# Optimization experiments

Measured on AMD Instinct MI355X. Metric: run time of the kernel, lower is better.

The kernel has to match this reference:

```python
import jax, jax.numpy as jnp
import numpy as np

HEADS = 8

def group_conv1x1(x, w, heads):
    # x: (B, Cin, H, W); w: (Cout, Cin//heads, 1, 1) grouped 1x1 conv, no bias
    B, Cin, H, W = x.shape
    Cout = w.shape[0]
    xg = x.reshape(B, heads, Cin // heads, H * W)
    wg = w[:, :, 0, 0].reshape(heads, Cout // heads, Cin // heads)
    out = jnp.einsum('hoc,bhcl->bhol', wg, xg)
    return out.reshape(B, Cout, H, W)

def sine_pe(d_model, length):
    # standard transformer sin/cos encoding, laid out as (d_model, length)
    pos = jnp.arange(length, dtype=jnp.float32)
    i = jnp.arange(0, d_model, 2, dtype=jnp.float32)
    div = jnp.exp(-(jnp.log(10000.0)) * i / d_model)
    ang = div[:, None] * pos[None, :]            # (d/2, L)
    pe = jnp.zeros((d_model, length), dtype=jnp.float32)
    pe = pe.at[0::2].set(jnp.sin(ang)).at[1::2].set(jnp.cos(ang))
    return pe

def setup_inputs() -> dict:
    key = jax.random.key(0)
    k0, k1, k2, k3 = jax.random.split(key, 4)
    B, Cin, H, W = 16, 256, 32, 32
    Cout, heads = 256, HEADS
    fan_out = Cout  # kaiming_normal fan_out for 1x1 conv = Cout*1*1
    std = np.sqrt(2.0 / fan_out)
    x = jax.random.normal(k0, (B, Cin, H, W), dtype=jnp.float32)
    wq = jax.random.normal(k1, (Cout, Cin // heads, 1, 1), dtype=jnp.float32) * std
    wk = jax.random.normal(k2, (Cout, Cin // heads, 1, 1), dtype=jnp.float32) * std
    wv = jax.random.normal(k3, (Cout, Cin // heads, 1, 1), dtype=jnp.float32) * std
    return {"x": x, "wq": wq, "wk": wk, "wv": wv}

def reference(x, wq, wk, wv):
    B, Cin, H, W = x.shape
    Cout = wq.shape[0]
    heads = HEADS
    dh = Cout // heads
    L = H * W

    q = group_conv1x1(x, wq, heads)              # (B, Cout, H, W)
    k = group_conv1x1(x, wk, heads)
    v = group_conv1x1(x, wv, heads)

    # sine positional encoding added to keys over flattened spatial positions
    k = k.reshape(B, Cout, L) + sine_pe(Cout, L)[None]

    q = q.reshape(B, heads, dh, L)               # (B, h, dh, L)
    k = k.reshape(B, heads, dh, L)
    v = v.reshape(B, heads, dh, L)

    scores = jnp.einsum('bhdq,bhdk->bhqk', q, k)  # (B, h, L, L) -- no sqrt(d) scaling, as in source
    attn = jax.nn.softmax(scores, axis=-1)
    out = jnp.einsum('bhqk,bhdk->bhdq', attn, v)  # (B, h, dh, L)
    return out.reshape(B, Cout, H, W)
```

## Files before the change

### kernel.cpp

```cpp
#include <hip/hip_runtime.h>

#define LL   1024
#define BHD  128
#define LOG2E 1.44269504088896340736f

typedef unsigned int       uint;
typedef unsigned short     ushort;
typedef unsigned long long ull;

typedef __attribute__((ext_vector_type(8)))  __bf16          bf16x8;
typedef __attribute__((ext_vector_type(8)))  unsigned short  u16x8;
typedef __attribute__((ext_vector_type(4)))  unsigned short  u16x4;
typedef __attribute__((ext_vector_type(4)))  uint            ui32x4;
typedef __attribute__((ext_vector_type(4)))  float           f32x4;
typedef __attribute__((ext_vector_type(16))) float           f32x16;

static __device__ __forceinline__ ushort f2bf(float f){
  union {float f; uint u;} v; v.f = f;
  uint u = v.u + 0x7fffu + ((v.u >> 16) & 1u);
  return (ushort)(u >> 16);
}
static __device__ __forceinline__ uint pack2(float a, float b){
  return (uint)f2bf(a) | ((uint)f2bf(b) << 16);
}
static __device__ __forceinline__ uint packtrunc(float a, float b){
  union {float f; uint u;} x, y; x.f = a; y.f = b;
  return __builtin_amdgcn_perm(y.u, x.u, 0x07060302u);
}
static __device__ __forceinline__ bf16x8 ld_frag(const ushort* p){
  u16x8 t = *(const u16x8*)p;
  return __builtin_bit_cast(bf16x8, t);
}
static __device__ __forceinline__ bf16x8 ld_frag64(const ushort* p){
  u16x4 a = *(const u16x4*)p;
  u16x4 b = *(const u16x4*)(p + 4);
  u16x8 t;
  t[0]=a[0]; t[1]=a[1]; t[2]=a[2]; t[3]=a[3];
  t[4]=b[0]; t[5]=b[1]; t[6]=b[2]; t[7]=b[3];
  return __builtin_bit_cast(bf16x8, t);
}

static __device__ __forceinline__ bool sniff_is_bf16(const uint* xw, int tid, int* cnt){
  uint w = xw[tid & 255];
  uint e = (w >> 7) & 0xFFu;
  bool hit = (e >= 118u) && (e <= 132u);
  ull b = __ballot(hit);
  if ((tid & 63) == 0) cnt[tid >> 6] = __popcll(b);
  __syncthreads();
  bool r = (cnt[0] + cnt[1] + cnt[2] + cnt[3]) > 128;
  __syncthreads();
  return r;
}

__global__ __launch_bounds__(256) void qkv_kernel(
    const void* __restrict__ xr,
    const void* __restrict__ wqr,
    const void* __restrict__ wkr,
    const void* __restrict__ wvr,
    ushort* __restrict__ Qt, ushort* __restrict__ Kt, ushort* __restrict__ Vt)
{
  const int bh   = blockIdx.x;
  const int lt   = blockIdx.y;
  const int tid  = threadIdx.x;
  const int wave = tid >> 6;
  const int lane = tid & 63;
  const int l16  = lane & 15;
  const int quad = lane >> 4;
  const int lbase = lt * 128;

  __shared__ int cnt[4];
  __shared__ __align__(16) uint xsd[128][20];

  const bool is_bf = sniff_is_bf16((const uint*)xr, tid, cnt);

  {
    const int cp = tid & 15, lg = tid >> 4;
    const size_t rb = (size_t)(bh*32 + 2*cp)*LL + lbase + lg*8;
    uint dw[8];
    if (is_bf){
      u16x8 e = *(const u16x8*)((const ushort*)xr + rb);
      u16x8 o = *(const u16x8*)((const ushort*)xr + rb + LL);
      #pragma unroll
      for (int j = 0; j < 8; ++j) dw[j] = (uint)e[j] | ((uint)o[j] << 16);
    } else {
      const float* xf = (const float*)xr;
      float4 e0 = *(const float4*)(xf + rb);
      float4 e1 = *(const float4*)(xf + rb + 4);
      float4 o0 = *(const float4*)(xf + rb + LL);
      float4 o1 = *(const float4*)(xf + rb + LL + 4);
      dw[0]=pack2(e0.x,o0.x); dw[1]=pack2(e0.y,o0.y);
      dw[2]=pack2(e0.z,o0.z); dw[3]=pack2(e0.w,o0.w);
      dw[4]=pack2(e1.x,o1.x); dw[5]=pack2(e1.y,o1.y);
      dw[6]=pack2(e1.z,o1.z); dw[7]=pack2(e1.w,o1.w);
    }
    #pragma unroll
    for (int j = 0; j < 8; ++j) xsd[lg*8 + j][cp] = dw[j];
  }
  __syncthreads();

  const void* wsrc[3] = {wqr, wkr, wvr};
  bf16x8 bw[3][2];
  #pragma unroll
  for (int p = 0; p < 3; ++p)
    #pragma unroll
    for (int nh = 0; nh < 2; ++nh){
      const int row = (bh & 7)*32 + nh*16 + l16;
      if (is_bf){
        bw[p][nh] = ld_frag((const ushort*)wsrc[p] + (size_t)row*32 + quad*8);
      } else {
        const float* wf = (const float*)wsrc[p] + (size_t)row*32 + quad*8;
        float4 f0 = *(const float4*)wf, f1 = *(const float4*)(wf + 4);
        u16x8 t;
        t[0]=f2bf(f0.x); t[1]=f2bf(f0.y); t[2]=f2bf(f0.z); t[3]=f2bf(f0.w);
        t[4]=f2bf(f1.x); t[5]=f2bf(f1.y); t[6]=f2bf(f1.z); t[7]=f2bf(f1.w);
        bw[p][nh] = __builtin_bit_cast(bf16x8, t);
      }
    }

  bf16x8 ax[2];
  #pragma unroll
  for (int mt = 0; mt < 2; ++mt)
    ax[mt] = __builtin_bit_cast(bf16x8,
               *(const ui32x4*)&xsd[wave*32 + mt*16 + l16][quad*4]);

  const f32x4 z = {0.f,0.f,0.f,0.f};
  f32x4 dq[2][2], dk[2][2], dv[2][2];
  #pragma unroll
  for (int mt = 0; mt < 2; ++mt)
    #pragma unroll
    for (int nh = 0; nh < 2; ++nh){
      dq[mt][nh] = __builtin_amdgcn_mfma_f32_16x16x32_bf16(ax[mt], bw[0][nh], z, 0,0,0);
      dk[mt][nh] = __builtin_amdgcn_mfma_f32_16x16x32_bf16(ax[mt], bw[1][nh], z, 0,0,0);
      dv[nh][mt] = __builtin_amdgcn_mfma_f32_16x16x32_bf16(bw[2][nh], ax[mt], z, 0,0,0);
    }

  #pragma unroll
  for (int mt = 0; mt < 2; ++mt)
    #pragma unroll
    for (int nh = 0; nh < 2; ++nh)
      #pragma unroll
      for (int r = 0; r < 4; ++r){
        const int l = lbase + wave*32 + mt*16 + quad*4 + r;
        const int d = nh*16 + l16;
        Qt[((size_t)bh*LL + l)*32 + d] = f2bf(dq[mt][nh][r]);
      }
  #pragma unroll
  for (int mt = 0; mt < 2; ++mt)
    #pragma unroll
    for (int nh = 0; nh < 2; ++nh){
      const int d = nh*16 + l16;
      const int c = (bh & 7)*32 + d;
      const float freq = __expf(-0.03597789207f * (float)(c & ~1));
      #pragma unroll
      for (int r = 0; r < 4; ++r){
        const int l = lbase + wave*32 + mt*16 + quad*4 + r;
        const float ang = freq * (float)l;
        const float pe  = (c & 1) ? __cosf(ang) : __sinf(ang);
        Kt[((size_t)bh*LL + l)*32 + d] = f2bf((dk[mt][nh][r] + pe) * LOG2E);
      }
    }
  #pragma unroll
  for (int dh = 0; dh < 2; ++dh)
    #pragma unroll
    for (int mt = 0; mt < 2; ++mt)
      #pragma unroll
      for (int r = 0; r < 4; ++r){
        const int d = dh*16 + quad*4 + r;
        const int l = lbase + wave*32 + mt*16 + l16;
        Vt[((size_t)(bh*32 + d))*LL + l] = f2bf(dv[dh][mt][r]);
      }
}

__global__ __launch_bounds__(256, 4) void attn_kernel(
    const void*   __restrict__ xr,
    const ushort* __restrict__ Qt,
    const ushort* __restrict__ Kt,
    const ushort* __restrict__ Vt,
    void* __restrict__ out)
{
  const int bh  = blockIdx.x;
  const int qt  = blockIdx.y;
  const int tid = threadIdx.x;
  const int wave = tid >> 6;
  const int lane = tid & 63;
  const int q32  = lane & 31;
  const int h    = lane >> 5;

  __shared__ int cnt[4];
  __shared__ __align__(16) ushort Ks[64][40];
  __shared__ __align__(16) ushort Vs[32][68];

  const bool is_bf = sniff_is_bf16((const uint*)xr, tid, cnt);

  const int qg = qt*128 + wave*32 + q32;
  const ushort* qrow = Qt + ((size_t)bh*LL + qg)*32;
  bf16x8 bq0 = ld_frag(qrow + h*8);
  bf16x8 bq1 = ld_frag(qrow + 16 + h*8);

  const int skey = tid >> 2, sseg = tid & 3;
  const int sp = (sseg + (skey >> 2)) & 3;
  const ushort* kg = Kt + ((size_t)(bh*LL + skey))*32 + sseg*8;
  ushort* kw = &Ks[skey][sp*8];
  const int sd = tid >> 3, sg = tid & 7;
  const ushort* vg = Vt + ((size_t)(bh*32 + sd))*LL + sg*8;
  ushort* vw = &Vs[sd][sg*8];

  const int rot = (q32 >> 2) & 3;
  const ushort* ka0 = &Ks[q32][((h + rot) & 3)*8];
  const ushort* ka1 = &Ks[q32][((2 + h + rot) & 3)*8];
  const ushort* vr  = &Vs[q32][h*8];

  f32x16 O = {};
  float rsum = 0.f;

  u16x8 kreg = *(const u16x8*)kg;
  u16x8 vreg = *(const u16x8*)vg;

  for (int kt = 0; kt < 16; ++kt){
    __syncthreads();
    *(u16x8*)kw = kreg;
    { u16x4 lo, hi;
      lo[0]=vreg[0]; lo[1]=vreg[1]; lo[2]=vreg[2]; lo[3]=vreg[3];
      hi[0]=vreg[4]; hi[1]=vreg[5]; hi[2]=vreg[6]; hi[3]=vreg[7];
      *(u16x4*)vw = lo; *(u16x4*)(vw + 4) = hi; }
    __syncthreads();
    if (kt < 15){
      kreg = *(const u16x8*)(kg + (size_t)(kt+1)*64*32);
      vreg = *(const u16x8*)(vg + (kt+1)*64);
    }

    f32x16 st[2];
    #pragma unroll
    for (int t = 0; t < 2; ++t){
      bf16x8 a0 = ld_frag(ka0 + t*32*40);
      bf16x8 a1 = ld_frag(ka1 + t*32*40);
      f32x16 zz = {};
      f32x16 s  = __builtin_amdgcn_mfma_f32_32x32x16_bf16(a0, bq0, zz, 0,0,0);
      st[t]     = __builtin_amdgcn_mfma_f32_32x32x16_bf16(a1, bq1, s,  0,0,0);
    }

    uint pr[2][8];
    #pragma unroll
    for (int t = 0; t < 2; ++t)
      #pragma unroll
      for (int zi = 0; zi < 8; ++zi){
        float p0 = __builtin_amdgcn_exp2f(st[t][2*zi]);
        float p1 = __builtin_amdgcn_exp2f(st[t][2*zi+1]);
        rsum += p0 + p1;
        pr[t][zi] = packtrunc(p0, p1);
      }

    #pragma unroll
    for (int c = 0; c < 4; ++c){
      const int t = c >> 1, g0 = 4*(c & 1);
      uint s0 = h ? pr[t][g0+0] : pr[t][g0+2];
      uint s1 = h ? pr[t][g0+1] : pr[t][g0+3];
      uint r0 = (uint)__shfl_xor((int)s0, 32);
      uint r1 = (uint)__shfl_xor((int)s1, 32);
      ui32x4 pb;
      pb[0] = h ? r0 : pr[t][g0+0];
      pb[1] = h ? r1 : pr[t][g0+1];
      pb[2] = h ? pr[t][g0+2] : r0;
      pb[3] = h ? pr[t][g0+3] : r1;
      bf16x8 va = ld_frag64(vr + c*16);
      O = __builtin_amdgcn_mfma_f32_32x32x16_bf16(
            va, __builtin_bit_cast(bf16x8, pb), O, 0,0,0);
    }
  }

  rsum += __shfl_xor(rsum, 32);
  const float inv = 1.f / rsum;

  #pragma unroll
  for (int reg = 0; reg < 16; ++reg){
    const int d = (reg & 3) + 8*(reg >> 2) + 4*h;
    const float v = O[reg] * inv;
    const size_t off = ((size_t)(bh*32 + d))*LL + qg;
    if (is_bf) ((ushort*)out)[off] = f2bf(v);
    else       ((float*)out)[off]  = v;
  }
}

extern "C" void kernel_launch(void* const* d_in, const int* in_sizes, int n_in,
                              void* d_out, int out_size, void* d_ws, size_t ws_size,
                              hipStream_t stream) {
  const void* x  = d_in[0];
  const void* wq = d_in[1];
  const void* wk = d_in[2];
  const void* wv = d_in[3];

  ushort* Qt = (ushort*)d_ws;
  ushort* Kt = Qt + (size_t)BHD * LL * 32;
  ushort* Vt = Kt + (size_t)BHD * LL * 32;

  qkv_kernel <<<dim3(BHD, 8), 256, 0, stream>>>(x, wq, wk, wv, Qt, Kt, Vt);
  attn_kernel<<<dim3(BHD, 8), 256, 0, stream>>>(x, Qt, Kt, Vt, d_out);
}
```

Baseline: 114.0 us.

## Store K/V in MFMA-fragment order and load directly from global, dropping LDS staging

The QKV projection now writes K and V in a tiled layout matching the attention kernel's MFMA operand fragments. It also uses packed 64-bit stores instead of scalar bf16 stores. The attention kernel drops its LDS staging of K/V tiles and the two barriers per iteration, and loads each fragment with a 16-byte global load. This removes shared-memory traffic and synchronisation, but relies on L2/cache reuse across the four waves that read the same K/V data, and the loads are no longer prefetched one tile ahead.

```diff
diff --git a/kernel.cpp b/kernel.cpp
--- a/kernel.cpp
+++ b/kernel.cpp
@@ -10,7 +10,7 @@
 
 typedef __attribute__((ext_vector_type(8)))  __bf16          bf16x8;
 typedef __attribute__((ext_vector_type(8)))  unsigned short  u16x8;
-typedef __attribute__((ext_vector_type(4)))  unsigned short  u16x4;
+typedef __attribute__((ext_vector_type(2)))  uint            ui32x2;
 typedef __attribute__((ext_vector_type(4)))  uint            ui32x4;
 typedef __attribute__((ext_vector_type(4)))  float           f32x4;
 typedef __attribute__((ext_vector_type(16))) float           f32x16;
@@ -29,14 +29,6 @@
 }
 static __device__ __forceinline__ bf16x8 ld_frag(const ushort* p){
   u16x8 t = *(const u16x8*)p;
-  return __builtin_bit_cast(bf16x8, t);
-}
-static __device__ __forceinline__ bf16x8 ld_frag64(const ushort* p){
-  u16x4 a = *(const u16x4*)p;
-  u16x4 b = *(const u16x4*)(p + 4);
-  u16x8 t;
-  t[0]=a[0]; t[1]=a[1]; t[2]=a[2]; t[3]=a[3];
-  t[4]=b[0]; t[5]=b[1]; t[6]=b[2]; t[7]=b[3];
   return __builtin_bit_cast(bf16x8, t);
 }
 
@@ -126,49 +118,60 @@
   const f32x4 z = {0.f,0.f,0.f,0.f};
   f32x4 dq[2][2], dk[2][2], dv[2][2];
   #pragma unroll
+  for (int nh = 0; nh < 2; ++nh)
+    #pragma unroll
+    for (int mt = 0; mt < 2; ++mt){
+      dq[nh][mt] = __builtin_amdgcn_mfma_f32_16x16x32_bf16(bw[0][nh], ax[mt], z, 0,0,0);
+      dk[nh][mt] = __builtin_amdgcn_mfma_f32_16x16x32_bf16(bw[1][nh], ax[mt], z, 0,0,0);
+      dv[mt][nh] = __builtin_amdgcn_mfma_f32_16x16x32_bf16(ax[mt], bw[2][nh], z, 0,0,0);
+    }
+
+  const int kt2   = lt*2 + (wave >> 1);
+  const size_t bhb = (size_t)bh * 32768;
+
+  #pragma unroll
+  for (int nh = 0; nh < 2; ++nh)
+    #pragma unroll
+    for (int mt = 0; mt < 2; ++mt){
+      const int l  = lbase + wave*32 + mt*16 + l16;
+      const int d0 = nh*16 + quad*4;
+      ui32x2 ww = { pack2(dq[nh][mt][0], dq[nh][mt][1]),
+                    pack2(dq[nh][mt][2], dq[nh][mt][3]) };
+      *(ui32x2*)&Qt[((size_t)bh*LL + l)*32 + d0] = ww;
+    }
+
+  #pragma unroll
+  for (int nh = 0; nh < 2; ++nh)
+    #pragma unroll
+    for (int mt = 0; mt < 2; ++mt){
+      const int l  = lbase + wave*32 + mt*16 + l16;
+      const int d0 = nh*16 + quad*4;
+      const int c0 = (bh & 7)*32 + d0;
+      const float fa = __expf(-0.03597789207f * (float)c0);
+      const float fb = __expf(-0.03597789207f * (float)(c0 + 2));
+      const float aa = fa * (float)l, ab = fb * (float)l;
+      const float k0 = (dk[nh][mt][0] + __sinf(aa)) * LOG2E;
+      const float k1 = (dk[nh][mt][1] + __cosf(aa)) * LOG2E;
+      const float k2 = (dk[nh][mt][2] + __sinf(ab)) * LOG2E;
+      const float k3 = (dk[nh][mt][3] + __cosf(ab)) * LOG2E;
+      const size_t off = bhb + (size_t)kt2*2048 + (size_t)(wave & 1)*1024
+                       + (size_t)nh*512 + (size_t)(quad >> 1)*256
+                       + (size_t)(mt*16 + l16)*8 + (quad & 1)*4;
+      ui32x2 ww = { pack2(k0, k1), pack2(k2, k3) };
+      *(ui32x2*)&Kt[off] = ww;
+    }
+
+  #pragma unroll
   for (int mt = 0; mt < 2; ++mt)
     #pragma unroll
-    for (int nh = 0; nh < 2; ++nh){
-      dq[mt][nh] = __builtin_amdgcn_mfma_f32_16x16x32_bf16(ax[mt], bw[0][nh], z, 0,0,0);
-      dk[mt][nh] = __builtin_amdgcn_mfma_f32_16x16x32_bf16(ax[mt], bw[1][nh], z, 0,0,0);
-      dv[nh][mt] = __builtin_amdgcn_mfma_f32_16x16x32_bf16(bw[2][nh], ax[mt], z, 0,0,0);
-    }
-
-  #pragma unroll
-  for (int mt = 0; mt < 2; ++mt)
-    #pragma unroll
-    for (int nh = 0; nh < 2; ++nh)
-      #pragma unroll
-      for (int r = 0; r < 4; ++r){
-        const int l = lbase + wave*32 + mt*16 + quad*4 + r;
-        const int d = nh*16 + l16;
-        Qt[((size_t)bh*LL + l)*32 + d] = f2bf(dq[mt][nh][r]);
-      }
-  #pragma unroll
-  for (int mt = 0; mt < 2; ++mt)
-    #pragma unroll
-    for (int nh = 0; nh < 2; ++nh){
-      const int d = nh*16 + l16;
-      const int c = (bh & 7)*32 + d;
-      const float freq = __expf(-0.03597789207f * (float)(c & ~1));
-      #pragma unroll
-      for (int r = 0; r < 4; ++r){
-        const int l = lbase + wave*32 + mt*16 + quad*4 + r;
-        const float ang = freq * (float)l;
-        const float pe  = (c & 1) ? __cosf(ang) : __sinf(ang);
-        Kt[((size_t)bh*LL + l)*32 + d] = f2bf((dk[mt][nh][r] + pe) * LOG2E);
-      }
-    }
-  #pragma unroll
-  for (int dh = 0; dh < 2; ++dh)
-    #pragma unroll
-    for (int mt = 0; mt < 2; ++mt)
-      #pragma unroll
-      for (int r = 0; r < 4; ++r){
-        const int d = dh*16 + quad*4 + r;
-        const int l = lbase + wave*32 + mt*16 + l16;
-        Vt[((size_t)(bh*32 + d))*LL + l] = f2bf(dv[dh][mt][r]);
-      }
+    for (int dh = 0; dh < 2; ++dh){
+      const size_t off = bhb + (size_t)kt2*2048 + (size_t)((wave*2 + mt) & 3)*512
+                       + (size_t)(quad >> 1)*256 + (size_t)(dh*16 + l16)*8
+                       + (quad & 1)*4;
+      ui32x2 ww = { pack2(dv[mt][dh][0], dv[mt][dh][1]),
+                    pack2(dv[mt][dh][2], dv[mt][dh][3]) };
+      *(ui32x2*)&Vt[off] = ww;
+    }
 }
 
 __global__ __launch_bounds__(256, 4) void attn_kernel(
@@ -187,9 +190,6 @@
   const int h    = lane >> 5;
 
   __shared__ int cnt[4];
-  __shared__ __align__(16) ushort Ks[64][40];
-  __shared__ __align__(16) ushort Vs[32][68];
-
   const bool is_bf = sniff_is_bf16((const uint*)xr, tid, cnt);
 
   const int qg = qt*128 + wave*32 + q32;
@@ -197,58 +197,45 @@
   bf16x8 bq0 = ld_frag(qrow + h*8);
   bf16x8 bq1 = ld_frag(qrow + 16 + h*8);
 
-  const int skey = tid >> 2, sseg = tid & 3;
-  const int sp = (sseg + (skey >> 2)) & 3;
-  const ushort* kg = Kt + ((size_t)(bh*LL + skey))*32 + sseg*8;
-  ushort* kw = &Ks[skey][sp*8];
-  const int sd = tid >> 3, sg = tid & 7;
-  const ushort* vg = Vt + ((size_t)(bh*32 + sd))*LL + sg*8;
-  ushort* vw = &Vs[sd][sg*8];
-
-  const int rot = (q32 >> 2) & 3;
-  const ushort* ka0 = &Ks[q32][((h + rot) & 3)*8];
-  const ushort* ka1 = &Ks[q32][((2 + h + rot) & 3)*8];
-  const ushort* vr  = &Vs[q32][h*8];
+  const ushort* kb = Kt + (size_t)bh*32768 + h*256 + q32*8;
+  const ushort* vb = Vt + (size_t)bh*32768 + h*256 + q32*8;
 
   f32x16 O = {};
   float rsum = 0.f;
 
-  u16x8 kreg = *(const u16x8*)kg;
-  u16x8 vreg = *(const u16x8*)vg;
-
   for (int kt = 0; kt < 16; ++kt){
-    __syncthreads();
-    *(u16x8*)kw = kreg;
-    { u16x4 lo, hi;
-      lo[0]=vreg[0]; lo[1]=vreg[1]; lo[2]=vreg[2]; lo[3]=vreg[3];
-      hi[0]=vreg[4]; hi[1]=vreg[5]; hi[2]=vreg[6]; hi[3]=vreg[7];
-      *(u16x4*)vw = lo; *(u16x4*)(vw + 4) = hi; }
-    __syncthreads();
-    if (kt < 15){
-      kreg = *(const u16x8*)(kg + (size_t)(kt+1)*64*32);
-      vreg = *(const u16x8*)(vg + (kt+1)*64);
-    }
+    const ushort* kp = kb + kt*2048;
+    const ushort* vp = vb + kt*2048;
+    bf16x8 k00 = ld_frag(kp);
+    bf16x8 k01 = ld_frag(kp + 512);
+    bf16x8 k10 = ld_frag(kp + 1024);
+    bf16x8 k11 = ld_frag(kp + 1536);
+    bf16x8 vf[4];
+    vf[0] = ld_frag(vp);
+    vf[1] = ld_frag(vp + 512);
+    vf[2] = ld_frag(vp + 1024);
+    vf[3] = ld_frag(vp + 1536);
 
     f32x16 st[2];
+    { f32x16 zz = {};
+      st[0] = __builtin_amdgcn_mfma_f32_32x32x16_bf16(k00, bq0, zz,    0,0,0);
+      st[0] = __builtin_amdgcn_mfma_f32_32x32x16_bf16(k01, bq1, st[0], 0,0,0);
+      st[1] = __builtin_amdgcn_mfma_f32_32x32x16_bf16(k10, bq0, zz,    0,0,0);
+      st[1] = __builtin_amdgcn_mfma_f32_32x32x16_bf16(k11, bq1, st[1], 0,0,0); }
+
+    uint pr[2][8];
     #pragma unroll
     for (int t = 0; t < 2; ++t){
-      bf16x8 a0 = ld_frag(ka0 + t*32*40);
-      bf16x8 a1 = ld_frag(ka1 + t*32*40);
-      f32x16 zz = {};
-      f32x16 s  = __builtin_amdgcn_mfma_f32_32x32x16_bf16(a0, bq0, zz, 0,0,0);
-      st[t]     = __builtin_amdgcn_mfma_f32_32x32x16_bf16(a1, bq1, s,  0,0,0);
-    }
-
-    uint pr[2][8];
-    #pragma unroll
-    for (int t = 0; t < 2; ++t)
+      float ts = 0.f;
       #pragma unroll
       for (int zi = 0; zi < 8; ++zi){
         float p0 = __builtin_amdgcn_exp2f(st[t][2*zi]);
         float p1 = __builtin_amdgcn_exp2f(st[t][2*zi+1]);
-        rsum += p0 + p1;
+        ts += p0 + p1;
         pr[t][zi] = packtrunc(p0, p1);
       }
+      rsum += ts;
+    }
 
     #pragma unroll
     for (int c = 0; c < 4; ++c){
@@ -262,9 +249,8 @@
       pb[1] = h ? r1 : pr[t][g0+1];
       pb[2] = h ? pr[t][g0+2] : r0;
       pb[3] = h ? pr[t][g0+3] : r1;
-      bf16x8 va = ld_frag64(vr + c*16);
       O = __builtin_amdgcn_mfma_f32_32x32x16_bf16(
-            va, __builtin_bit_cast(bf16x8, pb), O, 0,0,0);
+            vf[c], __builtin_bit_cast(bf16x8, pb), O, 0,0,0);
     }
   }
 
```

After: 112.6 us. Within noise of the previous version (-1.2%).
